# Performance work log

Measured on AMD Instinct MI355X. Metric: run time of the kernel, lower is better.

Reference implementation:

```python
import jax, jax.numpy as jnp
import numpy as np

NDIV = (10, 10)
OUT_CHANNEL = 100


def setup_inputs() -> dict:
    key = jax.random.key(0)
    k1, k2 = jax.random.split(key)
    x1 = jax.random.normal(k1, (8, 64, 128, 128), dtype=jnp.float32)
    x2 = jax.random.normal(k2, (8, 64, 60, 60), dtype=jnp.float32)
    return {"x1": x1, "x2": x2}


def reference(x1, x2):
    B, C, H, W = x1.shape
    h, w = x2.shape[-2], x2.shape[-1]
    nd0, nd1 = NDIV
    hh, ww = h // nd0, w // nd1  # patch size (6, 6)
    P = nd0 * nd1                # 100 patches per sample

    # channel-wise L2 normalization (dim=1)
    x1n = x1 / jnp.linalg.norm(x1, axis=1, keepdims=True)
    x2n = x2 / jnp.linalg.norm(x2, axis=1, keepdims=True)

    # extract nd0*nd1 patches per sample as conv filters: [B*P, C, hh, ww]
    patches = x2n.reshape(B, C, nd0, hh, nd1, ww)
    patches = patches.transpose(0, 2, 4, 1, 3, 5).reshape(B * P, C, hh, ww)

    # grouped cross-correlation (torch F.conv2d = correlation, no kernel flip)
    lhs = x1n.reshape(1, B * C, H, W)
    mm = jax.lax.conv_general_dilated(
        lhs, patches,
        window_strides=(1, 1),
        padding=((hh // 2, hh // 2), (ww // 2, ww // 2)),
        feature_group_count=B,
        dimension_numbers=("NCHW", "OIHW", "NCHW"),
    ) / (hh * ww)  # [1, B*P, H+1, W+1] for even hh,ww

    # bilinear resize to (H, W)  (torch align_corners=False == half-pixel)
    mm = jax.image.resize(mm, (1, B * P, H, W), method="bilinear")

    # [B, P, H, W] -> topk over patch dim, then mean
    mm = mm.reshape(B, P, H, W)
    topv = jax.lax.top_k(jnp.moveaxis(mm, 1, -1), OUT_CHANNEL)[0]  # [B,H,W,k]
    out = jnp.mean(topv, axis=-1)[:, None]  # [B,1,H,W]
    return out
```

## Files before the change

### kernel.cpp

```cpp
#include <hip/hip_runtime.h>
#include <cstddef>

#define BB   8
#define CC   64
#define H1   128
#define W1   128
#define HW1  (H1*W1)
#define HS   60
#define WS   60
#define HO   129
#define WO   129
#define NPIX (HS*WS)

#define UPL  (BB*HW1)

typedef _Float16 f16;

__global__ __launch_bounds__(256) void k_inv2(const float* __restrict__ x2,
                                              float* __restrict__ inv2) {
    int idx = blockIdx.x * 256 + threadIdx.x;
    if (idx >= BB * NPIX) return;
    int b  = idx / NPIX;
    int hw = idx - b * NPIX;
    const float* p = x2 + (size_t)b * CC * NPIX + hw;
    float s = 0.f;
#pragma unroll
    for (int cc = 0; cc < CC; cc += 8) {
        float v0 = p[(cc+0)*NPIX], v1 = p[(cc+1)*NPIX];
        float v2 = p[(cc+2)*NPIX], v3 = p[(cc+3)*NPIX];
        float v4 = p[(cc+4)*NPIX], v5 = p[(cc+5)*NPIX];
        float v6 = p[(cc+6)*NPIX], v7 = p[(cc+7)*NPIX];
        s += v0*v0 + v1*v1 + v2*v2 + v3*v3 + v4*v4 + v5*v5 + v6*v6 + v7*v7;
    }
    inv2[idx] = 1.0f / sqrtf(s);
}

__global__ __launch_bounds__(256) void k_fold(const float* __restrict__ x2,
                                              const float* __restrict__ inv2,
                                              float* __restrict__ S) {
    __shared__ float bins[36];
    int tid = threadIdx.x;
    int bc  = blockIdx.x;
    int b   = bc >> 6;
    if (tid < 36) bins[tid] = 0.f;
    __syncthreads();
    const float* px = x2 + (size_t)bc * NPIX;
    const float* pn = inv2 + b * NPIX;
    for (int i = tid; i < NPIX; i += 256) {
        int hh = i / WS, ww = i - hh * WS;
        int bin = (hh % 6) * 6 + (ww % 6);
        atomicAdd(&bins[bin], px[i] * pn[i]);
    }
    __syncthreads();
    if (tid < 36) S[bc * 36 + tid] = bins[tid];
}

__global__ __launch_bounds__(256) void k_gemm(const float* __restrict__ x1,
                                              const float* __restrict__ S,
                                              f16* __restrict__ U) {
    int b = blockIdx.x >> 6;
    int p = (blockIdx.x & 63) * 256 + threadIdx.x;

    const float* xp = x1 + (size_t)b * CC * HW1 + p;
    const float* Sb = S + (size_t)b * (CC * 36);

    float acc[36];
#pragma unroll
    for (int t = 0; t < 36; ++t) acc[t] = 0.f;
    float s2 = 0.f;

    for (int cc = 0; cc < CC; cc += 8) {
        float v[8];
#pragma unroll
        for (int j = 0; j < 8; ++j) v[j] = xp[(size_t)(cc + j) * HW1];
#pragma unroll
        for (int j = 0; j < 8; ++j) {
            const float* sj = Sb + (cc + j) * 36;
            float vv = v[j];
            s2 += vv * vv;
#pragma unroll
            for (int t = 0; t < 36; ++t) acc[t] += vv * sj[t];
        }
    }

    float inv = (1.0f / 3600.0f) / sqrtf(s2);
    f16* up = U + (size_t)b * HW1 + p;
#pragma unroll
    for (int t = 0; t < 36; ++t) up[(size_t)t * UPL] = (f16)(acc[t] * inv);
}

__global__ __launch_bounds__(256) void k_out(const f16* __restrict__ U,
                                             float* __restrict__ out) {
    __shared__ float m[20 * 21];
    int blk  = blockIdx.x;
    int b    = blk >> 6;
    int tile = blk & 63;
    int oy0 = (tile >> 3) * 16, ox0 = (tile & 7) * 16;
    int ry0 = oy0 - 1, rx0 = ox0 - 1;
    int tid = threadIdx.x;

    const f16* Ub = U + (size_t)b * HW1;

    for (int i = tid; i < 400; i += 256) {
        int ly = i / 20, lx = i - ly * 20;
        int jy = min(max(ry0 + ly, 0), 128);
        int jx = min(max(rx0 + lx, 0), 128);
        float s = 0.f;
#pragma unroll
        for (int t = 0; t < 36; ++t) {
            int dy = t / 6, dx = t - dy * 6;
            int py = jy - 3 + dy, px = jx - 3 + dx;
            if ((unsigned)py < 128u && (unsigned)px < 128u)
                s += (float)Ub[(size_t)t * UPL + py * W1 + px];
        }
        m[ly * 21 + lx] = s;
    }
    __syncthreads();

    const float inv_scale = 129.0f / 128.0f;
    const float ksc       = 128.0f / 129.0f;

    int oy = oy0 + (tid >> 4);
    int ox = ox0 + (tid & 15);

    float sy = (oy + 0.5f) * inv_scale - 0.5f;
    float sx = (ox + 0.5f) * inv_scale - 0.5f;
    int fy = (int)floorf(sy);
    int fx = (int)floorf(sx);

    float wy[4], wx[4];
    float sumy = 0.f, sumx = 0.f;
#pragma unroll
    for (int k = 0; k < 4; ++k) {
        int jy = fy - 1 + k;
        float w = 0.f;
        if (jy >= 0 && jy < HO) w = fmaxf(0.f, 1.0f - fabsf(sy - (float)jy) * ksc);
        wy[k] = w; sumy += w;
        int jx = fx - 1 + k;
        float w2 = 0.f;
        if (jx >= 0 && jx < WO) w2 = fmaxf(0.f, 1.0f - fabsf(sx - (float)jx) * ksc);
        wx[k] = w2; sumx += w2;
    }

    float r = 0.f;
#pragma unroll
    for (int ky = 0; ky < 4; ++ky) {
        if (wy[ky] == 0.f) continue;
        int ly = fy - 1 + ky - ry0;
        float rowv = 0.f;
#pragma unroll
        for (int kx = 0; kx < 4; ++kx) {
            if (wx[kx] == 0.f) continue;
            int lx = fx - 1 + kx - rx0;
            rowv += wx[kx] * m[ly * 21 + lx];
        }
        r += wy[ky] * rowv;
    }

    out[(size_t)b * HW1 + oy * W1 + ox] = r / (sumy * sumx);
}

extern "C" void kernel_launch(void* const* d_in, const int* in_sizes, int n_in,
                              void* d_out, int out_size, void* d_ws, size_t ws_size,
                              hipStream_t stream) {
    const float* x1 = (const float*)d_in[0];
    const float* x2 = (const float*)d_in[1];
    float* out = (float*)d_out;

    float* ws   = (float*)d_ws;
    float* inv2 = ws;
    float* Sbuf = inv2 + BB * NPIX;
    f16*   U    = (f16*)(Sbuf + BB * CC * 36);

    k_inv2<<<(BB * NPIX + 255) / 256, 256, 0, stream>>>(x2, inv2);
    k_fold<<<BB * CC, 256, 0, stream>>>(x2, inv2, Sbuf);
    k_gemm<<<BB * 64, 256, 0, stream>>>(x1, Sbuf, U);
    k_out <<<BB * 64, 256, 0, stream>>>(U, out);
}
```

Baseline: 129.3 us.

## Replace atomic binning in fold, remap block order, use nontemporal loads

The fold kernel now stages the normalized plane in shared memory with float4 loads and reduces each of the 36 bins with 7 threads and a tree sum, replacing the shared-memory atomics. The gemm and output kernels permute the block index so that consecutive blocks land on different batches, presumably to spread them across XCDs or channels. The x1 loads in gemm become nontemporal to avoid polluting the cache. The fold change removes atomic contention, while the remap and the nontemporal hint have uncertain effects on cache locality.

```diff
diff --git a/kernel.cpp b/kernel.cpp
--- a/kernel.cpp
+++ b/kernel.cpp
@@ -38,28 +38,49 @@
 __global__ __launch_bounds__(256) void k_fold(const float* __restrict__ x2,
                                               const float* __restrict__ inv2,
                                               float* __restrict__ S) {
-    __shared__ float bins[36];
+    __shared__ __align__(16) float pl[NPIX];
+    __shared__ float red[256];
     int tid = threadIdx.x;
     int bc  = blockIdx.x;
     int b   = bc >> 6;
-    if (tid < 36) bins[tid] = 0.f;
+
+    const float* px = x2 + (size_t)bc * NPIX;
+    const float* pn = inv2 + (size_t)b * NPIX;
+
+    const float4* px4 = (const float4*)px;
+    const float4* pn4 = (const float4*)pn;
+    float4* pl4 = (float4*)pl;
+    for (int i = tid; i < NPIX / 4; i += 256) {
+        float4 a = px4[i];
+        float4 w = pn4[i];
+        pl4[i] = make_float4(a.x * w.x, a.y * w.y, a.z * w.z, a.w * w.w);
+    }
     __syncthreads();
-    const float* px = x2 + (size_t)bc * NPIX;
-    const float* pn = inv2 + b * NPIX;
-    for (int i = tid; i < NPIX; i += 256) {
-        int hh = i / WS, ww = i - hh * WS;
-        int bin = (hh % 6) * 6 + (ww % 6);
-        atomicAdd(&bins[bin], px[i] * pn[i]);
-    }
+
+    float s = 0.f;
+    if (tid < 252) {
+        int bin = tid / 7, k = tid - bin * 7;
+        int r = bin / 6, c6 = bin - r * 6;
+        for (int e = k; e < 100; e += 7) {
+            int i = e / 10, j = e - i * 10;
+            s += pl[(r + 6 * i) * WS + (c6 + 6 * j)];
+        }
+    }
+    red[tid] = s;
     __syncthreads();
-    if (tid < 36) S[bc * 36 + tid] = bins[tid];
+
+    if (tid < 36) {
+        const float* q = red + tid * 7;
+        S[bc * 36 + tid] = q[0] + q[1] + q[2] + q[3] + q[4] + q[5] + q[6];
+    }
 }
 
 __global__ __launch_bounds__(256) void k_gemm(const float* __restrict__ x1,
                                               const float* __restrict__ S,
                                               f16* __restrict__ U) {
-    int b = blockIdx.x >> 6;
-    int p = (blockIdx.x & 63) * 256 + threadIdx.x;
+    int blk = (blockIdx.x & 7) * 64 + (blockIdx.x >> 3);
+    int b = blk >> 6;
+    int p = (blk & 63) * 256 + threadIdx.x;
 
     const float* xp = x1 + (size_t)b * CC * HW1 + p;
     const float* Sb = S + (size_t)b * (CC * 36);
@@ -72,7 +93,8 @@
     for (int cc = 0; cc < CC; cc += 8) {
         float v[8];
 #pragma unroll
-        for (int j = 0; j < 8; ++j) v[j] = xp[(size_t)(cc + j) * HW1];
+        for (int j = 0; j < 8; ++j)
+            v[j] = __builtin_nontemporal_load(&xp[(size_t)(cc + j) * HW1]);
 #pragma unroll
         for (int j = 0; j < 8; ++j) {
             const float* sj = Sb + (cc + j) * 36;
@@ -92,7 +114,7 @@
 __global__ __launch_bounds__(256) void k_out(const f16* __restrict__ U,
                                              float* __restrict__ out) {
     __shared__ float m[20 * 21];
-    int blk  = blockIdx.x;
+    int blk  = (blockIdx.x & 7) * 64 + (blockIdx.x >> 3);
     int b    = blk >> 6;
     int tile = blk & 63;
     int oy0 = (tile >> 3) * 16, ox0 = (tile & 7) * 16;
```

Measured after the change: 122.2 us. 5.5% less time.
